# Optimization experiments

Measured on AMD Instinct MI355X. Metric: run time of the kernel, lower is better.

## Reference

```python
import jax, jax.numpy as jnp
import numpy as np


def setup_inputs() -> dict:
    key = jax.random.key(0)
    ks = jax.random.split(key, 8)
    B, C, H, W = 16, 192, 64, 64
    dt_rank, d_state = 12, 1
    return {
        "x": jax.random.normal(ks[0], (B, C, H, W), dtype=jnp.float32),
        "conv_w": jax.random.normal(ks[1], (C, 1, 5, 5), dtype=jnp.float32) * 0.1,
        "conv_b": jax.random.normal(ks[2], (C,), dtype=jnp.float32) * 0.1,
        "x_proj_w": jax.random.normal(ks[3], (dt_rank + 2 * d_state, C), dtype=jnp.float32) * (C ** -0.5),
        "dt_w": jax.random.normal(ks[4], (C, dt_rank), dtype=jnp.float32) * (dt_rank ** -0.5),
        "dt_b": jax.random.normal(ks[5], (C,), dtype=jnp.float32) * 0.1,
        "A_logs": jnp.zeros((C, d_state), dtype=jnp.float32),  # log(arange(1,d_state+1)) with d_state=1 -> 0
        "Ds": jnp.ones((C,), dtype=jnp.float32),
    }


def reference(x, conv_w, conv_b, x_proj_w, dt_w, dt_b, A_logs, Ds):
    B, C, H, W = x.shape
    L = H * W
    dt_rank = dt_w.shape[1]
    n = A_logs.shape[1]  # d_state
    # depthwise conv2d, kernel 5, padding SAME (=d_conv//2), then SiLU
    x = jax.lax.conv_general_dilated(
        x, conv_w, window_strides=(1, 1), padding='SAME',
        feature_group_count=C, dimension_numbers=('NCHW', 'OIHW', 'NCHW'))
    x = jax.nn.silu(x + conv_b[None, :, None, None])
    xs = x.reshape(B, C, L)  # (b, d, l)
    # x_proj: (dt_rank + 2n, C) @ (b, C, l)
    x_dbl = jnp.einsum('kc,bcl->bkl', x_proj_w, xs)
    dts, Bs, Cs = jnp.split(x_dbl, [dt_rank, dt_rank + n], axis=1)
    # dt projection + softplus (delta_softplus=True with delta_bias)
    delta = jax.nn.softplus(jnp.einsum('cr,brl->bcl', dt_w, dts) + dt_b[None, :, None])  # (b,d,l)
    A = -jnp.exp(A_logs)  # (d, n)
    # selective scan returning the full state trajectory h_t (b,d,n,l):
    # h_t = exp(delta_t * A) * h_{t-1} + delta_t * B_t * u_t
    a = jnp.exp(delta[:, :, None, :] * A[None, :, :, None])        # (b,d,n,l)
    b_el = delta[:, :, None, :] * Bs[:, None, :, :] * xs[:, :, None, :]  # (b,d,n,l)

    def combine(e1, e2):
        a1, b1 = e1
        a2, b2 = e2
        return (a1 * a2, a2 * b1 + b2)

    _, h = jax.lax.associative_scan(combine, (a, b_el), axis=-1)  # h: (b,d,n,l)
    state = h.reshape(B, C * n, L)
    # y = C_t * h_t + D * u (fp32, d_state=1 broadcast)
    y = state.astype(jnp.float32) * Cs.astype(jnp.float32) + xs * Ds[:, None]
    return y.reshape(B, C, H, W)
```

## Files before the change

### kernel.cpp

```cpp
#include <hip/hip_runtime.h>
#include <hip/hip_bf16.h>
#include <cstddef>

#define BB 16
#define CC 192
#define HH 64
#define WW 64
#define LL 4096
#define DTR 12
#define KK 14

__device__ __forceinline__ float silu_f(float v) {
  return v / (1.f + __expf(-v));
}

__global__ __launch_bounds__(256) void conv_silu_kernel(
    const float* __restrict__ x, const float* __restrict__ cw,
    const float* __restrict__ cb, float* __restrict__ xs) {
  const int bc = blockIdx.x;
  const int c = bc % CC;
  const int tid = threadIdx.x;
  __shared__ float sm[68 * 72];

  const float* xp = x + (size_t)bc * LL;
  for (int i = tid; i < 68 * 72; i += 256) {
    int r = i / 72;
    int col = i - r * 72;
    int gy = r - 2, gx = col - 4;
    float v = 0.f;
    if ((unsigned)gy < 64u && (unsigned)gx < 64u) v = xp[gy * 64 + gx];
    sm[i] = v;
  }
  float w[25];
#pragma unroll
  for (int k = 0; k < 25; ++k) w[k] = cw[c * 25 + k];
  const float bias = cb[c];
  __syncthreads();

  float* op = xs + (size_t)bc * LL;
#pragma unroll
  for (int j = 0; j < 4; ++j) {
    const int quad = tid + j * 256;
    const int oy = quad >> 4;
    const int ox = (quad & 15) * 4;
    float acc[4] = {bias, bias, bias, bias};
#pragma unroll
    for (int ky = 0; ky < 5; ++ky) {
      const float4* smr = (const float4*)&sm[(oy + ky) * 72 + ox];
      float4 r0 = smr[0], r1 = smr[1], r2 = smr[2];
      float rw[12] = {r0.x, r0.y, r0.z, r0.w, r1.x, r1.y, r1.z, r1.w,
                      r2.x, r2.y, r2.z, r2.w};
#pragma unroll
      for (int kx = 0; kx < 5; ++kx) {
        float wv = w[ky * 5 + kx];
#pragma unroll
        for (int oi = 0; oi < 4; ++oi)
          acc[oi] += rw[2 + oi + kx] * wv;
      }
    }
    float4 o;
    o.x = silu_f(acc[0]);
    o.y = silu_f(acc[1]);
    o.z = silu_f(acc[2]);
    o.w = silu_f(acc[3]);
    *(float4*)(op + quad * 4) = o;
  }
}

__global__ __launch_bounds__(256) void proj_kernel(
    const float* __restrict__ xs, const float* __restrict__ xpw,
    float* __restrict__ xdbl) {
  const int b = blockIdx.y;
  const int l0 = blockIdx.x * 256;
  const int tid = threadIdx.x;
  const int lane = tid & 63;
  const int g = tid >> 6;

  __shared__ float part[4][KK][256];

  float4 acc[KK];
#pragma unroll
  for (int k = 0; k < KK; ++k) acc[k] = make_float4(0.f, 0.f, 0.f, 0.f);

  const float* bp = xs + ((size_t)(b * CC + g * 48)) * LL + l0 + lane * 4;
#pragma unroll 4
  for (int cc = 0; cc < 48; ++cc) {
    float4 v = *(const float4*)(bp + (size_t)cc * LL);
    const int c = g * 48 + cc;
#pragma unroll
    for (int k = 0; k < KK; ++k) {
      float wv = xpw[k * CC + c];
      acc[k].x += wv * v.x;
      acc[k].y += wv * v.y;
      acc[k].z += wv * v.z;
      acc[k].w += wv * v.w;
    }
  }
#pragma unroll
  for (int k = 0; k < KK; ++k)
    *(float4*)&part[g][k][lane * 4] = acc[k];
  __syncthreads();

  for (int idx = tid; idx < KK * 256; idx += 256) {
    int k = idx >> 8, ln = idx & 255;
    float v = part[0][k][ln] + part[1][k][ln] + part[2][k][ln] + part[3][k][ln];
    xdbl[((size_t)b * KK + k) * LL + l0 + ln] = v;
  }
}

__global__ __launch_bounds__(64) void scan_kernel(
    const float* __restrict__ xs, const float* __restrict__ xdbl,
    const float* __restrict__ dtw, const float* __restrict__ dtb,
    const float* __restrict__ A_logs, const float* __restrict__ Ds,
    float* __restrict__ y) {
  const int bc = blockIdx.x;
  const int b = bc / CC;
  const int c = bc - b * CC;
  const int lane = threadIdx.x;

  const float Ac = -__expf(A_logs[c]);
  const float Dc = Ds[c];
  float dw[DTR];
#pragma unroll
  for (int r = 0; r < DTR; ++r) dw[r] = dtw[c * DTR + r];
  const float db = dtb[c];

  const float* xp = xs + (size_t)bc * LL;
  const float* xb = xdbl + (size_t)b * KK * LL;
  float* yp = y + (size_t)bc * LL;

  float hcarry = 0.f;

  for (int sc = 0; sc < 16; ++sc) {
    const int base = sc * 256 + lane * 4;

    float4 x4 = *(const float4*)(xp + base);
    float4 B4 = *(const float4*)(xb + 12 * LL + base);
    float4 C4 = *(const float4*)(xb + 13 * LL + base);
    float4 dr[DTR];
#pragma unroll
    for (int r = 0; r < DTR; ++r)
      dr[r] = *(const float4*)(xb + r * LL + base);

    float xx[4] = {x4.x, x4.y, x4.z, x4.w};
    float bb[4] = {B4.x, B4.y, B4.z, B4.w};
    float av[4], bv[4];
    float aggA = 1.f, aggB = 0.f;
#pragma unroll
    for (int q = 0; q < 4; ++q) {
      float z = db;
#pragma unroll
      for (int r = 0; r < DTR; ++r) z += dw[r] * ((&dr[r].x)[q]);
      float delta = (z > 15.f) ? z : __logf(1.f + __expf(z));
      float a = __expf(delta * Ac);
      float be = delta * bb[q] * xx[q];
      av[q] = a;
      bv[q] = be;
      aggA = a * aggA;
      aggB = a * aggB + be;
    }

    float incA = aggA, incB = aggB;
#pragma unroll
    for (int s = 1; s < 64; s <<= 1) {
      float pA = __shfl_up(incA, (unsigned)s, 64);
      float pB = __shfl_up(incB, (unsigned)s, 64);
      if (lane >= s) {
        incB = incA * pB + incB;
        incA = incA * pA;
      }
    }
    float eA = __shfl_up(incA, 1u, 64);
    float eB = __shfl_up(incB, 1u, 64);
    if (lane == 0) { eA = 1.f; eB = 0.f; }
    float tA = __shfl(incA, 63, 64);
    float tB = __shfl(incB, 63, 64);

    float h = eA * hcarry + eB;
    float ov[4];
#pragma unroll
    for (int q = 0; q < 4; ++q) {
      h = av[q] * h + bv[q];
      ov[q] = h * ((&C4.x)[q]) + xx[q] * Dc;
    }
    float4 o;
    o.x = ov[0]; o.y = ov[1]; o.z = ov[2]; o.w = ov[3];
    *(float4*)(yp + base) = o;

    hcarry = tA * hcarry + tB;
  }
}

extern "C" void kernel_launch(void* const* d_in, const int* in_sizes, int n_in,
                              void* d_out, int out_size, void* d_ws,
                              size_t ws_size, hipStream_t stream) {
  const float* x        = (const float*)d_in[0];
  const float* conv_w   = (const float*)d_in[1];
  const float* conv_b   = (const float*)d_in[2];
  const float* x_proj_w = (const float*)d_in[3];
  const float* dt_w     = (const float*)d_in[4];
  const float* dt_b     = (const float*)d_in[5];
  const float* A_logs   = (const float*)d_in[6];
  const float* Ds       = (const float*)d_in[7];
  float* out = (float*)d_out;

  char* ws = (char*)d_ws;
  const size_t plane_bytes = (size_t)BB * CC * LL * sizeof(float);
  float* xs   = (float*)ws;
  float* xdbl = (float*)(ws + plane_bytes);

  conv_silu_kernel<<<dim3(BB * CC), 256, 0, stream>>>(x, conv_w, conv_b, xs);
  proj_kernel<<<dim3(LL / 256, BB), 256, 0, stream>>>(xs, x_proj_w, xdbl);
  scan_kernel<<<dim3(BB * CC), 64, 0, stream>>>(xs, xdbl, dt_w, dt_b,
                                                A_logs, Ds, out);
}
```

Baseline: 188.6 us.

## Rewrite depthwise conv as a single-wavefront row stream using lane shuffles

The depthwise 5x5 conv+SiLU kernel drops its 256-thread LDS-tiled version. Each block is now one 64-lane wavefront that streams the 64 rows of a plane, one column per lane. Horizontal neighbours come from cross-lane shuffles, and a 5-entry ring of row accumulators accumulates the vertical taps. This removes the shared-memory staging and the barrier. In exchange the work per plane becomes serial over rows, each block has a quarter of the threads, and the ring index must fold to a constant or it will spill to scratch.

```diff
diff --git a/kernel.cpp b/kernel.cpp
--- a/kernel.cpp
+++ b/kernel.cpp
@@ -14,56 +14,54 @@
   return v / (1.f + __expf(-v));
 }
 
-__global__ __launch_bounds__(256) void conv_silu_kernel(
+__global__ __launch_bounds__(64) void conv_silu_kernel(
     const float* __restrict__ x, const float* __restrict__ cw,
     const float* __restrict__ cb, float* __restrict__ xs) {
   const int bc = blockIdx.x;
   const int c = bc % CC;
-  const int tid = threadIdx.x;
-  __shared__ float sm[68 * 72];
-
-  const float* xp = x + (size_t)bc * LL;
-  for (int i = tid; i < 68 * 72; i += 256) {
-    int r = i / 72;
-    int col = i - r * 72;
-    int gy = r - 2, gx = col - 4;
-    float v = 0.f;
-    if ((unsigned)gy < 64u && (unsigned)gx < 64u) v = xp[gy * 64 + gx];
-    sm[i] = v;
-  }
+  const int lane = threadIdx.x;
+
   float w[25];
 #pragma unroll
   for (int k = 0; k < 25; ++k) w[k] = cw[c * 25 + k];
   const float bias = cb[c];
-  __syncthreads();
-
-  float* op = xs + (size_t)bc * LL;
-#pragma unroll
-  for (int j = 0; j < 4; ++j) {
-    const int quad = tid + j * 256;
-    const int oy = quad >> 4;
-    const int ox = (quad & 15) * 4;
-    float acc[4] = {bias, bias, bias, bias};
+
+  const float* xp = x + (size_t)bc * LL + lane;
+  float* op = xs + (size_t)bc * LL + lane;
+
+  float acc[5];
+#pragma unroll
+  for (int i = 0; i < 5; ++i) acc[i] = 0.f;
+
+#pragma unroll 5
+  for (int r = 0; r < 70; ++r) {
+    float v = 0.f;
+    if (r < 64) v = xp[r * 64];
+    float vm2 = __shfl_up(v, 2u, 64);
+    float vm1 = __shfl_up(v, 1u, 64);
+    float vp1 = __shfl_down(v, 1u, 64);
+    float vp2 = __shfl_down(v, 2u, 64);
+    if (lane < 2) vm2 = 0.f;
+    if (lane < 1) vm1 = 0.f;
+    if (lane > 62) vp1 = 0.f;
+    if (lane > 61) vp2 = 0.f;
+    float t[5] = {vm2, vm1, v, vp1, vp2};
 #pragma unroll
     for (int ky = 0; ky < 5; ++ky) {
-      const float4* smr = (const float4*)&sm[(oy + ky) * 72 + ox];
-      float4 r0 = smr[0], r1 = smr[1], r2 = smr[2];
-      float rw[12] = {r0.x, r0.y, r0.z, r0.w, r1.x, r1.y, r1.z, r1.w,
-                      r2.x, r2.y, r2.z, r2.w};
-#pragma unroll
-      for (int kx = 0; kx < 5; ++kx) {
-        float wv = w[ky * 5 + kx];
-#pragma unroll
-        for (int oi = 0; oi < 4; ++oi)
-          acc[oi] += rw[2 + oi + kx] * wv;
+      const int y = r - ky + 2;
+      if (y >= 0 && y < 64) {
+        float s = acc[y % 5];
+#pragma unroll
+        for (int kx = 0; kx < 5; ++kx) s += w[ky * 5 + kx] * t[kx];
+        acc[y % 5] = s;
       }
     }
-    float4 o;
-    o.x = silu_f(acc[0]);
-    o.y = silu_f(acc[1]);
-    o.z = silu_f(acc[2]);
-    o.w = silu_f(acc[3]);
-    *(float4*)(op + quad * 4) = o;
+    const int yf = r - 2;
+    if (yf >= 0 && yf < 64) {
+      float a = acc[yf % 5] + bias;
+      op[yf * 64] = silu_f(a);
+      acc[yf % 5] = 0.f;
+    }
   }
 }
 
@@ -209,7 +207,7 @@
   float* xs   = (float*)ws;
   float* xdbl = (float*)(ws + plane_bytes);
 
-  conv_silu_kernel<<<dim3(BB * CC), 256, 0, stream>>>(x, conv_w, conv_b, xs);
+  conv_silu_kernel<<<dim3(BB * CC), 64, 0, stream>>>(x, conv_w, conv_b, xs);
   proj_kernel<<<dim3(LL / 256, BB), 256, 0, stream>>>(xs, x_proj_w, xdbl);
   scan_kernel<<<dim3(BB * CC), 64, 0, stream>>>(xs, xdbl, dt_w, dt_b,
                                                 A_logs, Ds, out);
```

Result: slower. 199.5 us (+5.8%).
